# Kernel tuning notes

Hardware: AMD Instinct MI355X
Metric: run time of the kernel (lower is better)

The kernel has to match this reference:

```python
import jax, jax.numpy as jnp
import numpy as np

HIDDEN = 512
HEADS = 8


def setup_inputs() -> dict:
    key = jax.random.key(0)
    ks = jax.random.split(key, 7)
    B, S, D = 4, 2048, HIDDEN
    scale = 1.0 / np.sqrt(D)
    return {
        "src": jax.random.normal(ks[0], (B, S, D), dtype=jnp.float32),
        "Wq": jax.random.normal(ks[1], (D, D), dtype=jnp.float32) * scale,
        "bq": jax.random.normal(ks[2], (D,), dtype=jnp.float32) * 0.01,
        "Wk": jax.random.normal(ks[3], (D, D), dtype=jnp.float32) * scale,
        "bk": jax.random.normal(ks[4], (D,), dtype=jnp.float32) * 0.01,
        "Wv": jax.random.normal(ks[5], (D, D), dtype=jnp.float32) * scale,
        "bv": jax.random.normal(ks[6], (D,), dtype=jnp.float32) * 0.01,
    }


def reference(src, Wq, bq, Wk, bk, Wv, bv):
    B, S, D = src.shape
    H = HEADS
    hd = D // H
    # QKV projections -> [B, S, H, hd]
    q = (src @ Wq + bq).reshape(B, S, H, hd)
    k = (src @ Wk + bk).reshape(B, S, H, hd)
    v = (src @ Wv + bv).reshape(B, S, H, hd)
    # scores [B, H, S, S]; note: NO causal mask (matches original module)
    scores = jnp.einsum("bqhd,bkhd->bhqk", q, k) / jnp.sqrt(jnp.asarray(hd, src.dtype))
    attn = jax.nn.softmax(scores, axis=-1)
    out = jnp.einsum("bhqk,bkhd->bqhd", attn, v)
    return out.reshape(B, S, D)
```

## Files before the change

kernel.cpp:

```cpp
#include <hip/hip_runtime.h>

typedef __bf16 bf16;
typedef __bf16 bf16x8 __attribute__((ext_vector_type(8)));
typedef __bf16 bf16x4 __attribute__((ext_vector_type(4)));
typedef float f32x4 __attribute__((ext_vector_type(4)));
typedef float f32x16 __attribute__((ext_vector_type(16)));
typedef unsigned int u32;

#define QK_SCALE 0.1803368801111204f

__device__ __forceinline__ int swzb(int row, int col) {
    return (((row) << 7) + ((col) << 1)) ^ (((row) & 7) << 4);
}
__device__ __forceinline__ int kswz(int row, int g) {
    return row * 128 + ((g ^ (row & 7)) << 4);
}
__device__ __forceinline__ int vswz(int row, int g) {
    return row * 256 + ((g ^ (row & 15)) << 4);
}

__device__ __forceinline__ void gload_lds16(const void* g, void* l) {
    __builtin_amdgcn_global_load_lds(
        (const __attribute__((address_space(1))) unsigned int*)g,
        (__attribute__((address_space(3))) unsigned int*)l, 16, 0, 0);
}

__device__ __forceinline__ u32 cvtpk(float lo, float hi) {
    u32 r;
    asm("v_cvt_pk_bf16_f32 %0, %1, %2" : "=v"(r) : "v"(lo), "v"(hi));
    return r;
}
__device__ __forceinline__ void pl32swap(u32& a, u32& b) {
    asm("v_permlane32_swap_b32 %0, %1" : "+v"(a), "+v"(b));
}

__global__ __launch_bounds__(256) void cast_src(const float* __restrict__ x,
                                                bf16* __restrict__ y) {
    int i = blockIdx.x * 256 + threadIdx.x;
    float4 v = reinterpret_cast<const float4*>(x)[i];
    bf16x4 p;
    p[0] = (bf16)v.x; p[1] = (bf16)v.y; p[2] = (bf16)v.z; p[3] = (bf16)v.w;
    reinterpret_cast<bf16x4*>(y)[i] = p;
}

__global__ __launch_bounds__(256) void wtrans_all(const float* __restrict__ Wq,
                                                  const float* __restrict__ Wk,
                                                  const float* __restrict__ Wv,
                                                  bf16* __restrict__ Wt_all) {
    __shared__ float T[64][65];
    const int w = blockIdx.z;
    const float* W = w == 0 ? Wq : (w == 1 ? Wk : Wv);
    const float wsc = (w == 0) ? QK_SCALE : 1.0f;
    bf16* Wt = Wt_all + (size_t)w * 512 * 512;
    const int k0 = blockIdx.x * 64, n0 = blockIdx.y * 64;
    const int tx = threadIdx.x & 63, ty = threadIdx.x >> 6;
#pragma unroll
    for (int i = 0; i < 16; ++i) {
        int row = ty * 16 + i;
        T[row][tx] = W[(size_t)(k0 + row) * 512 + n0 + tx];
    }
    __syncthreads();
#pragma unroll
    for (int i = 0; i < 16; ++i) {
        int row = ty * 16 + i;
        Wt[(size_t)(n0 + row) * 512 + k0 + tx] = (bf16)(T[tx][row] * wsc);
    }
}

__global__ __launch_bounds__(256) void qkv_gemm_all(const bf16* __restrict__ srcb,
                                                    const bf16* __restrict__ Wt_all,
                                                    const float* __restrict__ bq,
                                                    const float* __restrict__ bk,
                                                    const float* __restrict__ bv,
                                                    bf16* __restrict__ Qb,
                                                    bf16* __restrict__ Kb,
                                                    bf16* __restrict__ Vtb) {
    __shared__ __align__(16) bf16 As[128 * 64];
    __shared__ __align__(16) bf16 Bs[128 * 64];
    const int t = threadIdx.x, lane = t & 63, wid = t >> 6;
    const int m0 = blockIdx.x * 128;
    const int n0g = blockIdx.y * 128;
    const int oi = n0g >> 9, n0 = n0g & 511;
    const float* bias = oi == 0 ? bq : (oi == 1 ? bk : bv);
    const float bsc = (oi == 0) ? QK_SCALE : 1.0f;
    bf16* outp = oi == 0 ? Qb : (oi == 1 ? Kb : Vtb);
    const bf16* Wt = Wt_all + (size_t)oi * 512 * 512;
    const bool sw = (oi == 2);
    const int wm = (wid >> 1) * 64, wn = (wid & 1) * 64;
    const int fr = lane & 15, fq = lane >> 4;

    f32x4 acc[4][4] = {};

    for (int k0 = 0; k0 < 512; k0 += 64) {
        __syncthreads();
#pragma unroll
        for (int c = 0; c < 4; ++c) {
            int u = (wid * 4 + c) * 64 + lane;
            int row = u >> 3;
            int slot = (u & 7) ^ (row & 7);
            gload_lds16(srcb + (size_t)(m0 + row) * 512 + k0 + slot * 8,
                        (char*)As + (wid * 4 + c) * 1024);
            gload_lds16(Wt + (size_t)(n0 + row) * 512 + k0 + slot * 8,
                        (char*)Bs + (wid * 4 + c) * 1024);
        }
        __syncthreads();

        bf16x8 a[2][4], b[2][4];
#pragma unroll
        for (int c = 0; c < 2; ++c)
#pragma unroll
            for (int i = 0; i < 4; ++i) {
                a[c][i] = *reinterpret_cast<const bf16x8*>(
                    (const char*)As + swzb(wm + i * 16 + fr, c * 32 + fq * 8));
                b[c][i] = *reinterpret_cast<const bf16x8*>(
                    (const char*)Bs + swzb(wn + i * 16 + fr, c * 32 + fq * 8));
            }
        if (!sw) {
#pragma unroll
            for (int i = 0; i < 4; ++i)
#pragma unroll
                for (int j = 0; j < 4; ++j)
#pragma unroll
                    for (int c = 0; c < 2; ++c)
                        acc[i][j] = __builtin_amdgcn_mfma_f32_16x16x32_bf16(a[c][i], b[c][j], acc[i][j], 0, 0, 0);
        } else {
#pragma unroll
            for (int i = 0; i < 4; ++i)
#pragma unroll
                for (int j = 0; j < 4; ++j)
#pragma unroll
                    for (int c = 0; c < 2; ++c)
                        acc[i][j] = __builtin_amdgcn_mfma_f32_16x16x32_bf16(b[c][j], a[c][i], acc[i][j], 0, 0, 0);
        }
    }

    if (!sw) {
#pragma unroll
        for (int j = 0; j < 4; ++j) {
            int n = n0 + wn + j * 16 + fr;
            float bj = bias[n] * bsc;
            int h = n >> 6, d = n & 63;
#pragma unroll
            for (int i = 0; i < 4; ++i)
#pragma unroll
                for (int r = 0; r < 4; ++r) {
                    int m = m0 + wm + i * 16 + fq * 4 + r;
                    int b_ = m >> 11, s = m & 2047;
                    outp[(((size_t)(b_ * 8 + h)) * 2048 + s) * 64 + d] =
                        (bf16)(acc[i][j][r] + bj);
                }
        }
    } else {
#pragma unroll
        for (int j = 0; j < 4; ++j)
#pragma unroll
            for (int r = 0; r < 4; ++r) {
                int n = n0 + wn + j * 16 + fq * 4 + r;
                float bj = bias[n];
                int h = n >> 6, d = n & 63;
#pragma unroll
                for (int i = 0; i < 4; ++i) {
                    int m = m0 + wm + i * 16 + fr;
                    int b_ = m >> 11, s = m & 2047;
                    outp[(((size_t)(b_ * 8 + h)) * 64 + d) * 2048 + s] =
                        (bf16)(acc[i][j][r] + bj);
                }
            }
    }
}

__global__ __launch_bounds__(256, 2) void attn_fwd(const bf16* __restrict__ Q,
                                                   const bf16* __restrict__ K,
                                                   const bf16* __restrict__ Vt,
                                                   float* __restrict__ out) {
    __shared__ __align__(16) bf16 Ks[2][128 * 64];
    __shared__ __align__(16) bf16 Vs[2][64 * 128];
    const int t = threadIdx.x, lane = t & 63, wid = t >> 6;
    const int c31 = lane & 31, h = lane >> 5;
    const int bh = blockIdx.y;
    const int qw = blockIdx.x * 128 + wid * 32;

    const bf16* Qp = Q + ((size_t)bh * 2048 + qw + c31) * 64;
    bf16x8 qf[4];
#pragma unroll
    for (int ks = 0; ks < 4; ++ks)
        qf[ks] = *reinterpret_cast<const bf16x8*>(&Qp[ks * 16 + h * 8]);

    bf16x8 bones;
#pragma unroll
    for (int e = 0; e < 8; ++e) bones[e] = (bf16)1.0f;

    f32x16 acc_o[2] = {};
    f32x16 acc_l = {};

    const char* Kpb0 = (const char*)(K + (size_t)bh * 2048 * 64);
    const char* Vpb0 = (const char*)(Vt + (size_t)bh * 64 * 2048);

    int koffs[4], voffs[4];
#pragma unroll
    for (int c = 0; c < 4; ++c) {
        int cc = wid * 4 + c;
        int kr = cc * 8 + (lane >> 3);
        koffs[c] = kr * 128 + (((lane & 7) ^ (kr & 7)) << 4);
        int d = cc * 4 + (lane >> 4);
        voffs[c] = d * 4096 + (((lane & 15) ^ (d & 15)) << 4);
    }

    auto stage = [&](int buf, int kv0) {
#pragma unroll
        for (int c = 0; c < 4; ++c)
            gload_lds16(Kpb0 + (size_t)kv0 * 128 + koffs[c],
                        (char*)Ks[buf] + (wid * 4 + c) * 1024);
#pragma unroll
        for (int c = 0; c < 4; ++c)
            gload_lds16(Vpb0 + (size_t)kv0 * 2 + voffs[c],
                        (char*)Vs[buf] + (wid * 4 + c) * 1024);
    };

    auto compute = [&](int buf) {
#pragma unroll
        for (int p = 0; p < 2; ++p) {
            f32x16 s0 = {}, s1 = {};
            __builtin_amdgcn_s_setprio(1);
#pragma unroll
            for (int ks = 0; ks < 4; ++ks) {
                bf16x8 kf0 = *reinterpret_cast<const bf16x8*>(
                    (const char*)Ks[buf] + kswz(p * 64 + c31, ks * 2 + h));
                s0 = __builtin_amdgcn_mfma_f32_32x32x16_bf16(kf0, qf[ks], s0, 0, 0, 0);
                bf16x8 kf1 = *reinterpret_cast<const bf16x8*>(
                    (const char*)Ks[buf] + kswz(p * 64 + 32 + c31, ks * 2 + h));
                s1 = __builtin_amdgcn_mfma_f32_32x32x16_bf16(kf1, qf[ks], s1, 0, 0, 0);
            }
            __builtin_amdgcn_s_setprio(0);

#pragma unroll
            for (int r = 0; r < 16; ++r) {
                s0[r] = __builtin_amdgcn_exp2f(s0[r]);
                s1[r] = __builtin_amdgcn_exp2f(s1[r]);
            }

            bf16x8 pa[4];
#pragma unroll
            for (int ktl = 0; ktl < 2; ++ktl) {
                const f32x16& sv = ktl ? s1 : s0;
#pragma unroll
                for (int k2 = 0; k2 < 2; ++k2) {
                    u32 X = cvtpk(sv[8 * k2 + 0], sv[8 * k2 + 1]);
                    u32 Y = cvtpk(sv[8 * k2 + 4], sv[8 * k2 + 5]);
                    u32 Z = cvtpk(sv[8 * k2 + 2], sv[8 * k2 + 3]);
                    u32 W = cvtpk(sv[8 * k2 + 6], sv[8 * k2 + 7]);
                    pl32swap(X, Y);
                    pl32swap(Z, W);
                    union { bf16x8 v; u32 w[4]; } pu;
                    pu.w[0] = X; pu.w[1] = Z; pu.w[2] = Y; pu.w[3] = W;
                    pa[ktl * 2 + k2] = pu.v;
                }
            }

            __builtin_amdgcn_s_setprio(1);
#pragma unroll
            for (int k2 = 0; k2 < 4; ++k2) {
                int kg = p * 4 + k2;
                bf16x8 vf0 = *reinterpret_cast<const bf16x8*>(
                    (const char*)Vs[buf] + vswz(c31, kg * 2 + h));
                acc_o[0] = __builtin_amdgcn_mfma_f32_32x32x16_bf16(pa[k2], vf0, acc_o[0], 0, 0, 0);
                bf16x8 vf1 = *reinterpret_cast<const bf16x8*>(
                    (const char*)Vs[buf] + vswz(32 + c31, kg * 2 + h));
                acc_o[1] = __builtin_amdgcn_mfma_f32_32x32x16_bf16(pa[k2], vf1, acc_o[1], 0, 0, 0);
                acc_l = __builtin_amdgcn_mfma_f32_32x32x16_bf16(pa[k2], bones, acc_l, 0, 0, 0);
            }
            __builtin_amdgcn_s_setprio(0);
        }
    };

    stage(0, 0);
    __syncthreads();

    for (int kv0 = 0; kv0 < 2048; kv0 += 256) {
        stage(1, kv0 + 128);
        compute(0);
        __syncthreads();
        if (kv0 + 256 < 2048) stage(0, kv0 + 256);
        compute(1);
        __syncthreads();
    }

    const int b_ = bh >> 3, hh = bh & 7;
#pragma unroll
    for (int reg = 0; reg < 16; ++reg) {
        float inv = __builtin_amdgcn_rcpf(acc_l[reg]);
        int qr = (reg & 3) + 8 * (reg >> 2) + 4 * h;
        int s_ = qw + qr;
        size_t base = ((size_t)b_ * 2048 + s_) * 512 + hh * 64;
        out[base + c31]      = acc_o[0][reg] * inv;
        out[base + 32 + c31] = acc_o[1][reg] * inv;
    }
}

extern "C" void kernel_launch(void* const* d_in, const int* in_sizes, int n_in,
                              void* d_out, int out_size, void* d_ws, size_t ws_size,
                              hipStream_t stream) {
    const float* src = (const float*)d_in[0];
    const float* Wq  = (const float*)d_in[1];
    const float* bq  = (const float*)d_in[2];
    const float* Wk  = (const float*)d_in[3];
    const float* bk  = (const float*)d_in[4];
    const float* Wv  = (const float*)d_in[5];
    const float* bv  = (const float*)d_in[6];
    float* out = (float*)d_out;

    char* ws = (char*)d_ws;
    const size_t WT_SZ  = 512u * 512u * sizeof(bf16);
    const size_t QKV_SZ = 8192u * 512u * sizeof(bf16);
    bf16* WtA  = (bf16*)(ws);
    bf16* srcb = (bf16*)(ws + 3 * WT_SZ);
    bf16* Qb   = (bf16*)(ws + 3 * WT_SZ + QKV_SZ);
    bf16* Kb   = (bf16*)(ws + 3 * WT_SZ + 2 * QKV_SZ);
    bf16* Vtb  = (bf16*)(ws + 3 * WT_SZ + 3 * QKV_SZ);

    cast_src<<<4096, 256, 0, stream>>>(src, srcb);
    wtrans_all<<<dim3(8, 8, 3), 256, 0, stream>>>(Wq, Wk, Wv, WtA);

    qkv_gemm_all<<<dim3(64, 12), 256, 0, stream>>>(srcb, WtA, bq, bk, bv, Qb, Kb, Vtb);

    attn_fwd<<<dim3(16, 32), 256, 0, stream>>>(Qb, Kb, Vtb, out);
}
```

Baseline: 80.02 us.

## Split attention KV range across two wave groups with LDS reduction

Doubles the attention block to 512 threads. The two 4-wave groups each process half of the key/value sequence over the same 128 queries, using 64-row KV tiles with a new swizzled LDS layout. At the end, group 1 writes its partial output and row sums to LDS, and group 0 adds them and normalizes. This is meant to raise the number of waves in flight and hide latency, at the cost of an extra LDS reduction and a change in occupancy limits. It relies on there being no running max, so the partial sums can simply be added.

```diff
diff --git a/kernel.cpp b/kernel.cpp
--- a/kernel.cpp
+++ b/kernel.cpp
@@ -9,14 +9,11 @@
 
 #define QK_SCALE 0.1803368801111204f
 
+__device__ __forceinline__ int rc16(int row, int g) {
+    return row * 256 + ((g ^ (row & 15)) << 4);
+}
 __device__ __forceinline__ int swzb(int row, int col) {
     return (((row) << 7) + ((col) << 1)) ^ (((row) & 7) << 4);
-}
-__device__ __forceinline__ int kswz(int row, int g) {
-    return row * 128 + ((g ^ (row & 7)) << 4);
-}
-__device__ __forceinline__ int vswz(int row, int g) {
-    return row * 256 + ((g ^ (row & 15)) << 4);
 }
 
 __device__ __forceinline__ void gload_lds16(const void* g, void* l) {
@@ -169,16 +166,16 @@
     }
 }
 
-__global__ __launch_bounds__(256, 2) void attn_fwd(const bf16* __restrict__ Q,
+__global__ __launch_bounds__(512, 4) void attn_fwd(const bf16* __restrict__ Q,
                                                    const bf16* __restrict__ K,
                                                    const bf16* __restrict__ Vt,
                                                    float* __restrict__ out) {
-    __shared__ __align__(16) bf16 Ks[2][128 * 64];
-    __shared__ __align__(16) bf16 Vs[2][64 * 128];
+    __shared__ __align__(16) char lds_raw[65536];
     const int t = threadIdx.x, lane = t & 63, wid = t >> 6;
+    const int grp = wid >> 2, w4 = wid & 3;
     const int c31 = lane & 31, h = lane >> 5;
     const int bh = blockIdx.y;
-    const int qw = blockIdx.x * 128 + wid * 32;
+    const int qw = blockIdx.x * 128 + w4 * 32;
 
     const bf16* Qp = Q + ((size_t)bh * 2048 + qw + c31) * 64;
     bf16x8 qf[4];
@@ -196,104 +193,116 @@
     const char* Kpb0 = (const char*)(K + (size_t)bh * 2048 * 64);
     const char* Vpb0 = (const char*)(Vt + (size_t)bh * 64 * 2048);
 
-    int koffs[4], voffs[4];
-#pragma unroll
-    for (int c = 0; c < 4; ++c) {
-        int cc = wid * 4 + c;
-        int kr = cc * 8 + (lane >> 3);
-        koffs[c] = kr * 128 + (((lane & 7) ^ (kr & 7)) << 4);
-        int d = cc * 4 + (lane >> 4);
-        voffs[c] = d * 4096 + (((lane & 15) ^ (d & 15)) << 4);
-    }
-
-    auto stage = [&](int buf, int kv0) {
-#pragma unroll
-        for (int c = 0; c < 4; ++c)
-            gload_lds16(Kpb0 + (size_t)kv0 * 128 + koffs[c],
-                        (char*)Ks[buf] + (wid * 4 + c) * 1024);
-#pragma unroll
-        for (int c = 0; c < 4; ++c)
-            gload_lds16(Vpb0 + (size_t)kv0 * 2 + voffs[c],
-                        (char*)Vs[buf] + (wid * 4 + c) * 1024);
+    auto stage = [&](int buf, int tt) {
+        const size_t kv0 = (size_t)(grp * 1024 + tt * 64);
+        const char* Kg = Kpb0 + kv0 * 128;
+        const char* Vg = Vpb0 + kv0 * 2;
+        char* Kl = lds_raw + (grp * 2 + buf) * 8192;
+        char* Vl = lds_raw + 32768 + (grp * 2 + buf) * 8192;
+#pragma unroll
+        for (int c = 0; c < 2; ++c) {
+            int ch = w4 * 2 + c;
+            int r = ch * 4 + (lane >> 4);
+            int g = (lane & 15) ^ (r & 15);
+            gload_lds16(Kg + r * 256 + g * 16, Kl + ch * 1024);
+            gload_lds16(Vg + (size_t)(2 * r + (g >> 3)) * 4096 + (g & 7) * 16,
+                        Vl + ch * 1024);
+        }
     };
 
     auto compute = [&](int buf) {
-#pragma unroll
-        for (int p = 0; p < 2; ++p) {
-            f32x16 s0 = {}, s1 = {};
-            __builtin_amdgcn_s_setprio(1);
-#pragma unroll
-            for (int ks = 0; ks < 4; ++ks) {
-                bf16x8 kf0 = *reinterpret_cast<const bf16x8*>(
-                    (const char*)Ks[buf] + kswz(p * 64 + c31, ks * 2 + h));
-                s0 = __builtin_amdgcn_mfma_f32_32x32x16_bf16(kf0, qf[ks], s0, 0, 0, 0);
-                bf16x8 kf1 = *reinterpret_cast<const bf16x8*>(
-                    (const char*)Ks[buf] + kswz(p * 64 + 32 + c31, ks * 2 + h));
-                s1 = __builtin_amdgcn_mfma_f32_32x32x16_bf16(kf1, qf[ks], s1, 0, 0, 0);
+        const char* Kl = lds_raw + (grp * 2 + buf) * 8192;
+        const char* Vl = lds_raw + 32768 + (grp * 2 + buf) * 8192;
+        const int rq = c31 >> 1, gb = (c31 & 1) * 8;
+
+        f32x16 s0 = {}, s1 = {};
+        __builtin_amdgcn_s_setprio(1);
+#pragma unroll
+        for (int ks = 0; ks < 4; ++ks) {
+            int g = gb + ks * 2 + h;
+            bf16x8 kf0 = *reinterpret_cast<const bf16x8*>(Kl + rc16(rq, g));
+            s0 = __builtin_amdgcn_mfma_f32_32x32x16_bf16(kf0, qf[ks], s0, 0, 0, 0);
+            bf16x8 kf1 = *reinterpret_cast<const bf16x8*>(Kl + rc16(16 + rq, g));
+            s1 = __builtin_amdgcn_mfma_f32_32x32x16_bf16(kf1, qf[ks], s1, 0, 0, 0);
+        }
+        __builtin_amdgcn_s_setprio(0);
+
+#pragma unroll
+        for (int r = 0; r < 16; ++r) {
+            s0[r] = __builtin_amdgcn_exp2f(s0[r]);
+            s1[r] = __builtin_amdgcn_exp2f(s1[r]);
+        }
+
+        bf16x8 pa[4];
+#pragma unroll
+        for (int ktl = 0; ktl < 2; ++ktl) {
+            const f32x16& sv = ktl ? s1 : s0;
+#pragma unroll
+            for (int k2 = 0; k2 < 2; ++k2) {
+                u32 X = cvtpk(sv[8 * k2 + 0], sv[8 * k2 + 1]);
+                u32 Y = cvtpk(sv[8 * k2 + 4], sv[8 * k2 + 5]);
+                u32 Z = cvtpk(sv[8 * k2 + 2], sv[8 * k2 + 3]);
+                u32 W = cvtpk(sv[8 * k2 + 6], sv[8 * k2 + 7]);
+                pl32swap(X, Y);
+                pl32swap(Z, W);
+                union { bf16x8 v; u32 w[4]; } pu;
+                pu.w[0] = X; pu.w[1] = Z; pu.w[2] = Y; pu.w[3] = W;
+                pa[ktl * 2 + k2] = pu.v;
             }
-            __builtin_amdgcn_s_setprio(0);
-
-#pragma unroll
-            for (int r = 0; r < 16; ++r) {
-                s0[r] = __builtin_amdgcn_exp2f(s0[r]);
-                s1[r] = __builtin_amdgcn_exp2f(s1[r]);
-            }
-
-            bf16x8 pa[4];
-#pragma unroll
-            for (int ktl = 0; ktl < 2; ++ktl) {
-                const f32x16& sv = ktl ? s1 : s0;
-#pragma unroll
-                for (int k2 = 0; k2 < 2; ++k2) {
-                    u32 X = cvtpk(sv[8 * k2 + 0], sv[8 * k2 + 1]);
-                    u32 Y = cvtpk(sv[8 * k2 + 4], sv[8 * k2 + 5]);
-                    u32 Z = cvtpk(sv[8 * k2 + 2], sv[8 * k2 + 3]);
-                    u32 W = cvtpk(sv[8 * k2 + 6], sv[8 * k2 + 7]);
-                    pl32swap(X, Y);
-                    pl32swap(Z, W);
-                    union { bf16x8 v; u32 w[4]; } pu;
-                    pu.w[0] = X; pu.w[1] = Z; pu.w[2] = Y; pu.w[3] = W;
-                    pa[ktl * 2 + k2] = pu.v;
-                }
-            }
-
-            __builtin_amdgcn_s_setprio(1);
-#pragma unroll
-            for (int k2 = 0; k2 < 4; ++k2) {
-                int kg = p * 4 + k2;
-                bf16x8 vf0 = *reinterpret_cast<const bf16x8*>(
-                    (const char*)Vs[buf] + vswz(c31, kg * 2 + h));
-                acc_o[0] = __builtin_amdgcn_mfma_f32_32x32x16_bf16(pa[k2], vf0, acc_o[0], 0, 0, 0);
-                bf16x8 vf1 = *reinterpret_cast<const bf16x8*>(
-                    (const char*)Vs[buf] + vswz(32 + c31, kg * 2 + h));
-                acc_o[1] = __builtin_amdgcn_mfma_f32_32x32x16_bf16(pa[k2], vf1, acc_o[1], 0, 0, 0);
-                acc_l = __builtin_amdgcn_mfma_f32_32x32x16_bf16(pa[k2], bones, acc_l, 0, 0, 0);
-            }
-            __builtin_amdgcn_s_setprio(0);
-        }
+        }
+
+        __builtin_amdgcn_s_setprio(1);
+#pragma unroll
+        for (int kg = 0; kg < 4; ++kg) {
+            int g = gb + kg * 2 + h;
+            bf16x8 vf0 = *reinterpret_cast<const bf16x8*>(Vl + rc16(rq, g));
+            acc_o[0] = __builtin_amdgcn_mfma_f32_32x32x16_bf16(pa[kg], vf0, acc_o[0], 0, 0, 0);
+            bf16x8 vf1 = *reinterpret_cast<const bf16x8*>(Vl + rc16(16 + rq, g));
+            acc_o[1] = __builtin_amdgcn_mfma_f32_32x32x16_bf16(pa[kg], vf1, acc_o[1], 0, 0, 0);
+            acc_l = __builtin_amdgcn_mfma_f32_32x32x16_bf16(pa[kg], bones, acc_l, 0, 0, 0);
+        }
+        __builtin_amdgcn_s_setprio(0);
     };
 
     stage(0, 0);
     __syncthreads();
 
-    for (int kv0 = 0; kv0 < 2048; kv0 += 256) {
-        stage(1, kv0 + 128);
+    for (int tt = 0; tt < 16; tt += 2) {
+        stage(1, tt + 1);
         compute(0);
         __syncthreads();
-        if (kv0 + 256 < 2048) stage(0, kv0 + 256);
+        if (tt + 2 < 16) stage(0, tt + 2);
         compute(1);
         __syncthreads();
     }
 
-    const int b_ = bh >> 3, hh = bh & 7;
-#pragma unroll
-    for (int reg = 0; reg < 16; ++reg) {
-        float inv = __builtin_amdgcn_rcpf(acc_l[reg]);
-        int qr = (reg & 3) + 8 * (reg >> 2) + 4 * h;
-        int s_ = qw + qr;
-        size_t base = ((size_t)b_ * 2048 + s_) * 512 + hh * 64;
-        out[base + c31]      = acc_o[0][reg] * inv;
-        out[base + 32 + c31] = acc_o[1][reg] * inv;
+    float* Os = (float*)lds_raw;
+    float* Ls = (float*)(lds_raw + 32768);
+    if (grp == 1) {
+#pragma unroll
+        for (int dt = 0; dt < 2; ++dt)
+#pragma unroll
+            for (int reg = 0; reg < 16; ++reg)
+                Os[(((w4 * 2 + dt) * 16 + reg) * 2 + h) * 32 + c31] = acc_o[dt][reg];
+#pragma unroll
+        for (int reg = 0; reg < 16; ++reg)
+            Ls[(w4 * 16 + reg) * 64 + lane] = acc_l[reg];
+    }
+    __syncthreads();
+    if (grp == 0) {
+        const int b_ = bh >> 3, hh = bh & 7;
+#pragma unroll
+        for (int reg = 0; reg < 16; ++reg) {
+            float l = acc_l[reg] + Ls[(w4 * 16 + reg) * 64 + lane];
+            float inv = __builtin_amdgcn_rcpf(l);
+            int qr = (reg & 3) + 8 * (reg >> 2) + 4 * h;
+            int s_ = qw + qr;
+            size_t base = ((size_t)b_ * 2048 + s_) * 512 + hh * 64;
+            out[base + c31] =
+                (acc_o[0][reg] + Os[(((w4 * 2 + 0) * 16 + reg) * 2 + h) * 32 + c31]) * inv;
+            out[base + 32 + c31] =
+                (acc_o[1][reg] + Os[(((w4 * 2 + 1) * 16 + reg) * 2 + h) * 32 + c31]) * inv;
+        }
     }
 }
 
@@ -323,5 +332,5 @@
 
     qkv_gemm_all<<<dim3(64, 12), 256, 0, stream>>>(srcb, WtA, bq, bk, bv, Qb, Kb, Vtb);
 
-    attn_fwd<<<dim3(16, 32), 256, 0, stream>>>(Qb, Kb, Vtb, out);
-}
+    attn_fwd<<<dim3(16, 32), 512, 0, stream>>>(Qb, Kb, Vtb, out);
+}
```

Result: slower. 82.44 us (+3.0%).
